# Kernel tuning notes

Hardware: AMD Instinct MI355X
Metric: run time of the kernel (lower is better)

The kernel has to match this reference:

```python
import jax, jax.numpy as jnp
import numpy as np

H, DK = 16, 128  # heads, head dim; d_model = H*DK = 2048

def setup_inputs() -> dict:
    key0 = jax.random.key(0)
    ks = jax.random.split(key0, 11)
    B, S, D = 8, 4096, H * DK
    s = 1.0 / np.sqrt(D)
    return {
        "query": jax.random.normal(ks[0], (B, D), jnp.float32),
        "key": jax.random.normal(ks[1], (S, B, D), jnp.float32),
        "value": jax.random.normal(ks[2], (S, B, D), jnp.float32),
        "Wq": jax.random.normal(ks[3], (D, D), jnp.float32) * s,
        "Wk": jax.random.normal(ks[4], (D, D), jnp.float32) * s,
        "Wv": jax.random.normal(ks[5], (D, D), jnp.float32) * s,
        "bv": jax.random.normal(ks[6], (D,), jnp.float32) * 0.01,
        "Wo": jax.random.normal(ks[7], (D, D), jnp.float32) * s,
        "bo": jax.random.normal(ks[8], (D,), jnp.float32) * 0.01,
        "key_pos": jax.random.normal(ks[9], (4096, H, DK), jnp.float32) * 0.02,
        "q_bias": jax.random.normal(ks[10], (H, DK), jnp.float32) * 0.02,
    }

def reference(query, key, value, Wq, Wk, Wv, bv, Wo, bo, key_pos, q_bias):
    S, B, D = key.shape
    scale = 1.0 / jnp.sqrt(jnp.asarray(DK, query.dtype))
    q = (query @ Wq).reshape(B, H, DK)                 # [B,H,DK]
    k = (key.reshape(S * B, D) @ Wk).reshape(S, B, H, DK)
    v = (value.reshape(S * B, D) @ Wv + bv).reshape(S, B, H, DK)
    kp = key_pos[-S:]                                  # [S,H,DK]
    scores = jnp.einsum('bhd,jbhd->jbh', q + q_bias, k + kp[:, None]) * scale
    attn = jax.nn.softmax(scores, axis=0)              # softmax over seq (dim 0)
    x = jnp.einsum('jbh,jbhd->bhd', attn, v).reshape(B, D)
    return x @ Wo + bo
```

## Files before the change

### kernel.cpp

```cpp
#include <hip/hip_runtime.h>

#define B 8
#define S 4096
#define H 16
#define DK 128
#define D 2048
#define SCALE 0.08838834764831845f

__global__ __launch_bounds__(256) void k0_init(float* __restrict__ qq, float* __restrict__ U,
                                               float* __restrict__ x, float* __restrict__ out,
                                               const float* __restrict__ q_bias,
                                               const float* __restrict__ bv,
                                               const float* __restrict__ bo) {
    int idx = blockIdx.x * 256 + threadIdx.x;
    if (idx < B * D) {
        int d = idx & (D - 1);
        qq[idx]  = q_bias[d];
        x[idx]   = bv[d];
        out[idx] = bo[d];
    }
    if (idx < B * H * D) U[idx] = 0.f;
}

__global__ __launch_bounds__(256) void k1_qproj(const float* __restrict__ query,
                                                const float* __restrict__ Wq,
                                                float* __restrict__ qq) {
    int dout = blockIdx.x * 256 + threadIdx.x;
    int e0 = blockIdx.y * 64;
    float acc[B] = {};
    #pragma unroll 4
    for (int e = e0; e < e0 + 64; ++e) {
        float w = Wq[(size_t)e * D + dout];
        #pragma unroll
        for (int b = 0; b < B; ++b) acc[b] = fmaf(query[b * D + e], w, acc[b]);
    }
    #pragma unroll
    for (int b = 0; b < B; ++b) atomicAdd(&qq[b * D + dout], acc[b]);
}

__global__ __launch_bounds__(256) void k2_A(const float* __restrict__ Wk,
                                            const float* __restrict__ qq,
                                            float* __restrict__ A) {
    int h = blockIdx.x;
    int e = blockIdx.y * 256 + threadIdx.x;
    const float* wrow = Wk + (size_t)e * D + h * DK;
    const float* qb = qq + h * DK;
    float acc[B] = {};
    #pragma unroll 4
    for (int t = 0; t < DK / 4; ++t) {
        float4 w = *(const float4*)(wrow + 4 * t);
        #pragma unroll
        for (int b = 0; b < B; ++b) {
            const float* q4 = qb + b * D + 4 * t;
            acc[b] += w.x * q4[0] + w.y * q4[1] + w.z * q4[2] + w.w * q4[3];
        }
    }
    #pragma unroll
    for (int b = 0; b < B; ++b) A[((size_t)b * H + h) * D + e] = acc[b];
}

__global__ __launch_bounds__(256) void kq_pos(const float* __restrict__ key_pos,
                                              const float* __restrict__ qq,
                                              float* __restrict__ scores) {
    int tid = threadIdx.x;
    int lane = tid & 63;
    int wave = tid >> 6;
    int lane31 = lane & 31;
    int half = lane >> 5;
    for (int t = 0; t < 16; ++t) {
        int task = (blockIdx.x * 4 + wave) * 16 + t;
        int j = task >> 3;
        int hh = task & 7;
        float4 kp4 = *(const float4*)(key_pos + (size_t)j * D + hh * 256 + lane * 4);
        int h = hh * 2 + half;
        #pragma unroll
        for (int b = 0; b < B; ++b) {
            float4 q4 = *(const float4*)(qq + (size_t)b * D + hh * 256 + lane * 4);
            float v = kp4.x * q4.x + kp4.y * q4.y + kp4.z * q4.z + kp4.w * q4.w;
            v += __shfl_xor(v, 1, 64);
            v += __shfl_xor(v, 2, 64);
            v += __shfl_xor(v, 4, 64);
            v += __shfl_xor(v, 8, 64);
            v += __shfl_xor(v, 16, 64);
            if (lane31 == 0) scores[((size_t)b * H + h) * S + j] = v;
        }
    }
}

#define TJ 64
#define EC 128
#define ECF4 32
#define KST 33
__global__ __launch_bounds__(256) void k3_scores(const float* __restrict__ key,
                                                 const float* __restrict__ A,
                                                 float* __restrict__ scores) {
    __shared__ float4 klds[TJ * KST];
    int tid = threadIdx.x;
    int b = blockIdx.y;
    int j0 = blockIdx.x * TJ;
    int jslot = tid & 63;
    int h0 = __builtin_amdgcn_readfirstlane((tid >> 6) << 2);
    const float* Ab = A + ((size_t)b * H + h0) * D;
    float acc0 = 0.f, acc1 = 0.f, acc2 = 0.f, acc3 = 0.f;

    int srow = tid >> 5;
    int scol = tid & 31;
    for (int s = 0; s < D / EC; ++s) {
        __syncthreads();
        const float* gp = key + ((size_t)(j0 + srow) * B + b) * D + s * EC + scol * 4;
        #pragma unroll
        for (int p = 0; p < 8; ++p) {
            klds[(srow + p * 8) * KST + scol] = *(const float4*)(gp + (size_t)p * 8 * B * D);
        }
        __syncthreads();
        const float* Ac = Ab + s * EC;
        #pragma unroll 8
        for (int c = 0; c < ECF4; ++c) {
            float4 k4 = klds[jslot * KST + c];
            float4 a0 = *(const float4*)(Ac + 0 * D + c * 4);
            float4 a1 = *(const float4*)(Ac + 1 * D + c * 4);
            float4 a2 = *(const float4*)(Ac + 2 * D + c * 4);
            float4 a3 = *(const float4*)(Ac + 3 * D + c * 4);
            acc0 += k4.x * a0.x + k4.y * a0.y + k4.z * a0.z + k4.w * a0.w;
            acc1 += k4.x * a1.x + k4.y * a1.y + k4.z * a1.z + k4.w * a1.w;
            acc2 += k4.x * a2.x + k4.y * a2.y + k4.z * a2.z + k4.w * a2.w;
            acc3 += k4.x * a3.x + k4.y * a3.y + k4.z * a3.z + k4.w * a3.w;
        }
    }
    float* sp = scores + ((size_t)b * H + h0) * S + j0 + jslot;
    sp[0 * S] += acc0;
    sp[1 * S] += acc1;
    sp[2 * S] += acc2;
    sp[3 * S] += acc3;
}

__global__ __launch_bounds__(256) void k4_softmax(float* __restrict__ scores) {
    int bh = blockIdx.x;
    float* row = scores + (size_t)bh * S;
    __shared__ float red[4];
    int tid = threadIdx.x, lane = tid & 63, w = tid >> 6;
    float m = -3.0e38f;
    for (int i = tid; i < S; i += 256) m = fmaxf(m, row[i]);
    #pragma unroll
    for (int o = 32; o; o >>= 1) m = fmaxf(m, __shfl_xor(m, o, 64));
    if (lane == 0) red[w] = m;
    __syncthreads();
    float M = fmaxf(fmaxf(red[0], red[1]), fmaxf(red[2], red[3]));
    __syncthreads();
    float s = 0.f;
    for (int i = tid; i < S; i += 256) {
        float e = __expf((row[i] - M) * SCALE);
        row[i] = e;
        s += e;
    }
    #pragma unroll
    for (int o = 32; o; o >>= 1) s += __shfl_xor(s, o, 64);
    if (lane == 0) red[w] = s;
    __syncthreads();
    float inv = 1.f / (red[0] + red[1] + red[2] + red[3]);
    for (int i = tid; i < S; i += 256) row[i] *= inv;
}

__global__ __launch_bounds__(512) void k5_U(const float* __restrict__ value,
                                            const float* __restrict__ attn,
                                            float* __restrict__ U) {
    int tid = threadIdx.x;
    int b = blockIdx.y;
    int j0 = blockIdx.x * 128;
    const float* vbase = value + ((size_t)j0 * B + b) * D + tid * 4;
    float4 acc[H];
    #pragma unroll
    for (int h = 0; h < H; ++h) acc[h] = make_float4(0.f, 0.f, 0.f, 0.f);
    for (int jj = 0; jj < 128; jj += 4) {
        float4 v0 = *(const float4*)(vbase + (size_t)(jj + 0) * B * D);
        float4 v1 = *(const float4*)(vbase + (size_t)(jj + 1) * B * D);
        float4 v2 = *(const float4*)(vbase + (size_t)(jj + 2) * B * D);
        float4 v3 = *(const float4*)(vbase + (size_t)(jj + 3) * B * D);
        #pragma unroll
        for (int h = 0; h < H; ++h) {
            float4 wv = *(const float4*)(attn + ((size_t)b * H + h) * S + j0 + jj);
            acc[h].x += wv.x * v0.x + wv.y * v1.x + wv.z * v2.x + wv.w * v3.x;
            acc[h].y += wv.x * v0.y + wv.y * v1.y + wv.z * v2.y + wv.w * v3.y;
            acc[h].z += wv.x * v0.z + wv.y * v1.z + wv.z * v2.z + wv.w * v3.z;
            acc[h].w += wv.x * v0.w + wv.y * v1.w + wv.z * v2.w + wv.w * v3.w;
        }
    }
    float* ub = U + (size_t)b * H * D + tid * 4;
    #pragma unroll
    for (int h = 0; h < H; ++h) {
        atomicAdd(ub + h * D + 0, acc[h].x);
        atomicAdd(ub + h * D + 1, acc[h].y);
        atomicAdd(ub + h * D + 2, acc[h].z);
        atomicAdd(ub + h * D + 3, acc[h].w);
    }
}

__global__ __launch_bounds__(128) void k6_xv(const float* __restrict__ Wv,
                                             const float* __restrict__ U,
                                             float* __restrict__ x) {
    int d = threadIdx.x;
    int h = blockIdx.y;
    int e0 = blockIdx.x * 32;
    float acc[B] = {};
    #pragma unroll 4
    for (int ee = 0; ee < 32; ++ee) {
        int e = e0 + ee;
        float w = Wv[(size_t)e * D + h * DK + d];
        #pragma unroll
        for (int b = 0; b < B; ++b)
            acc[b] = fmaf(U[((size_t)b * H + h) * D + e], w, acc[b]);
    }
    #pragma unroll
    for (int b = 0; b < B; ++b) atomicAdd(&x[b * D + h * DK + d], acc[b]);
}

__global__ __launch_bounds__(256) void k7_out(const float* __restrict__ x,
                                              const float* __restrict__ Wo,
                                              float* __restrict__ out) {
    int dout = blockIdx.x * 256 + threadIdx.x;
    int e0 = blockIdx.y * 64;
    float acc[B] = {};
    #pragma unroll 4
    for (int e = e0; e < e0 + 64; ++e) {
        float w = Wo[(size_t)e * D + dout];
        #pragma unroll
        for (int b = 0; b < B; ++b) acc[b] = fmaf(x[b * D + e], w, acc[b]);
    }
    #pragma unroll
    for (int b = 0; b < B; ++b) atomicAdd(&out[b * D + dout], acc[b]);
}

extern "C" void kernel_launch(void* const* d_in, const int* in_sizes, int n_in,
                              void* d_out, int out_size, void* d_ws, size_t ws_size,
                              hipStream_t stream) {
    const float* query   = (const float*)d_in[0];
    const float* key     = (const float*)d_in[1];
    const float* value   = (const float*)d_in[2];
    const float* Wq      = (const float*)d_in[3];
    const float* Wk      = (const float*)d_in[4];
    const float* Wv      = (const float*)d_in[5];
    const float* bv      = (const float*)d_in[6];
    const float* Wo      = (const float*)d_in[7];
    const float* bo      = (const float*)d_in[8];
    const float* key_pos = (const float*)d_in[9];
    const float* q_bias  = (const float*)d_in[10];
    float* out = (float*)d_out;

    float* ws     = (float*)d_ws;
    float* qq     = ws;
    float* A      = ws + 16384;
    float* scores = ws + 278528;
    float* U      = ws + 802816;
    float* x      = ws + 1064960;

    hipLaunchKernelGGL(k0_init,    dim3(1024),      dim3(256), 0, stream, qq, U, x, out, q_bias, bv, bo);
    hipLaunchKernelGGL(k1_qproj,   dim3(8, 32),     dim3(256), 0, stream, query, Wq, qq);
    hipLaunchKernelGGL(k2_A,       dim3(16, 8),     dim3(256), 0, stream, Wk, qq, A);
    hipLaunchKernelGGL(kq_pos,     dim3(512),       dim3(256), 0, stream, key_pos, qq, scores);
    hipLaunchKernelGGL(k3_scores,  dim3(64, 8),     dim3(256), 0, stream, key, A, scores);
    hipLaunchKernelGGL(k4_softmax, dim3(128),       dim3(256), 0, stream, scores);
    hipLaunchKernelGGL(k5_U,       dim3(32, 8),     dim3(512), 0, stream, value, scores, U);
    hipLaunchKernelGGL(k6_xv,      dim3(64, 16),    dim3(128), 0, stream, Wv, U, x);
    hipLaunchKernelGGL(k7_out,     dim3(8, 32),     dim3(256), 0, stream, x, Wo, out);
}
```

Before: 894.3 us.

## Replace k5 atomics with partial buffers plus reduction; recast k2_A as wave-per-row

The value-weighted accumulation kernel now writes per-sequence-tile partial sums to a workspace buffer, and a new reduction kernel sums them. This removes the global atomics and the zero-init of U, and the tile count is picked from the available workspace size. Separately, the Wk·q kernel is reorganised so each wave handles one row of Wk with coalesced float4 loads and shuffle reductions, instead of each thread striding across a row. In exchange it adds an extra kernel launch and extra partial-buffer traffic, and with a small workspace the tile count can be low, which limits parallelism.

```diff
diff --git a/kernel.cpp b/kernel.cpp
--- a/kernel.cpp
+++ b/kernel.cpp
@@ -7,7 +7,7 @@
 #define D 2048
 #define SCALE 0.08838834764831845f
 
-__global__ __launch_bounds__(256) void k0_init(float* __restrict__ qq, float* __restrict__ U,
+__global__ __launch_bounds__(256) void k0_init(float* __restrict__ qq,
                                                float* __restrict__ x, float* __restrict__ out,
                                                const float* __restrict__ q_bias,
                                                const float* __restrict__ bv,
@@ -19,7 +19,6 @@
         x[idx]   = bv[d];
         out[idx] = bo[d];
     }
-    if (idx < B * H * D) U[idx] = 0.f;
 }
 
 __global__ __launch_bounds__(256) void k1_qproj(const float* __restrict__ query,
@@ -41,22 +40,27 @@
 __global__ __launch_bounds__(256) void k2_A(const float* __restrict__ Wk,
                                             const float* __restrict__ qq,
                                             float* __restrict__ A) {
-    int h = blockIdx.x;
-    int e = blockIdx.y * 256 + threadIdx.x;
-    const float* wrow = Wk + (size_t)e * D + h * DK;
-    const float* qb = qq + h * DK;
-    float acc[B] = {};
-    #pragma unroll 4
-    for (int t = 0; t < DK / 4; ++t) {
-        float4 w = *(const float4*)(wrow + 4 * t);
+    int tid = threadIdx.x;
+    int lane = tid & 63, wave = tid >> 6;
+    int lane31 = lane & 31, half = lane >> 5;
+    int e = blockIdx.x * 4 + wave;
+    const float* wrow = Wk + (size_t)e * D;
+    #pragma unroll
+    for (int p = 0; p < 8; ++p) {
+        float4 w4 = *(const float4*)(wrow + p * 256 + lane * 4);
+        int h = p * 2 + half;
         #pragma unroll
         for (int b = 0; b < B; ++b) {
-            const float* q4 = qb + b * D + 4 * t;
-            acc[b] += w.x * q4[0] + w.y * q4[1] + w.z * q4[2] + w.w * q4[3];
-        }
-    }
-    #pragma unroll
-    for (int b = 0; b < B; ++b) A[((size_t)b * H + h) * D + e] = acc[b];
+            float4 q4 = *(const float4*)(qq + (size_t)b * D + p * 256 + lane * 4);
+            float v = w4.x * q4.x + w4.y * q4.y + w4.z * q4.z + w4.w * q4.w;
+            v += __shfl_xor(v, 1, 64);
+            v += __shfl_xor(v, 2, 64);
+            v += __shfl_xor(v, 4, 64);
+            v += __shfl_xor(v, 8, 64);
+            v += __shfl_xor(v, 16, 64);
+            if (lane31 == 0) A[((size_t)b * H + h) * D + e] = v;
+        }
+    }
 }
 
 __global__ __launch_bounds__(256) void kq_pos(const float* __restrict__ key_pos,
@@ -163,15 +167,16 @@
 
 __global__ __launch_bounds__(512) void k5_U(const float* __restrict__ value,
                                             const float* __restrict__ attn,
-                                            float* __restrict__ U) {
+                                            float* __restrict__ Upart, int jlen) {
     int tid = threadIdx.x;
     int b = blockIdx.y;
-    int j0 = blockIdx.x * 128;
+    int jt = blockIdx.x;
+    int j0 = jt * jlen;
     const float* vbase = value + ((size_t)j0 * B + b) * D + tid * 4;
     float4 acc[H];
     #pragma unroll
     for (int h = 0; h < H; ++h) acc[h] = make_float4(0.f, 0.f, 0.f, 0.f);
-    for (int jj = 0; jj < 128; jj += 4) {
+    for (int jj = 0; jj < jlen; jj += 4) {
         float4 v0 = *(const float4*)(vbase + (size_t)(jj + 0) * B * D);
         float4 v1 = *(const float4*)(vbase + (size_t)(jj + 1) * B * D);
         float4 v2 = *(const float4*)(vbase + (size_t)(jj + 2) * B * D);
@@ -185,14 +190,21 @@
             acc[h].w += wv.x * v0.w + wv.y * v1.w + wv.z * v2.w + wv.w * v3.w;
         }
     }
-    float* ub = U + (size_t)b * H * D + tid * 4;
-    #pragma unroll
-    for (int h = 0; h < H; ++h) {
-        atomicAdd(ub + h * D + 0, acc[h].x);
-        atomicAdd(ub + h * D + 1, acc[h].y);
-        atomicAdd(ub + h * D + 2, acc[h].z);
-        atomicAdd(ub + h * D + 3, acc[h].w);
-    }
+    float* ub = Upart + (((size_t)jt * B + b) * H) * D + tid * 4;
+    #pragma unroll
+    for (int h = 0; h < H; ++h) *(float4*)(ub + (size_t)h * D) = acc[h];
+}
+
+__global__ __launch_bounds__(256) void k5r(const float* __restrict__ Upart,
+                                           float* __restrict__ U, int JT) {
+    int i = blockIdx.x * 256 + threadIdx.x;
+    float4 s = make_float4(0.f, 0.f, 0.f, 0.f);
+    #pragma unroll 4
+    for (int t = 0; t < JT; ++t) {
+        float4 p = *(const float4*)(Upart + (size_t)t * (B * H * D) + (size_t)i * 4);
+        s.x += p.x; s.y += p.y; s.z += p.z; s.w += p.w;
+    }
+    *(float4*)(U + (size_t)i * 4) = s;
 }
 
 __global__ __launch_bounds__(128) void k6_xv(const float* __restrict__ Wv,
@@ -252,14 +264,23 @@
     float* scores = ws + 278528;
     float* U      = ws + 802816;
     float* x      = ws + 1064960;
-
-    hipLaunchKernelGGL(k0_init,    dim3(1024),      dim3(256), 0, stream, qq, U, x, out, q_bias, bv, bo);
+    float* Upart  = ws + 1081344;
+
+    int JT = 1;
+    for (int cand = 64; cand >= 1; cand >>= 1) {
+        size_t need = ((size_t)1081344 + (size_t)cand * 262144) * sizeof(float);
+        if (need <= ws_size) { JT = cand; break; }
+    }
+    int jlen = S / JT;
+
+    hipLaunchKernelGGL(k0_init,    dim3(64),        dim3(256), 0, stream, qq, x, out, q_bias, bv, bo);
     hipLaunchKernelGGL(k1_qproj,   dim3(8, 32),     dim3(256), 0, stream, query, Wq, qq);
-    hipLaunchKernelGGL(k2_A,       dim3(16, 8),     dim3(256), 0, stream, Wk, qq, A);
+    hipLaunchKernelGGL(k2_A,       dim3(512),       dim3(256), 0, stream, Wk, qq, A);
     hipLaunchKernelGGL(kq_pos,     dim3(512),       dim3(256), 0, stream, key_pos, qq, scores);
     hipLaunchKernelGGL(k3_scores,  dim3(64, 8),     dim3(256), 0, stream, key, A, scores);
     hipLaunchKernelGGL(k4_softmax, dim3(128),       dim3(256), 0, stream, scores);
-    hipLaunchKernelGGL(k5_U,       dim3(32, 8),     dim3(512), 0, stream, value, scores, U);
+    hipLaunchKernelGGL(k5_U,       dim3(JT, 8),     dim3(512), 0, stream, value, scores, Upart, jlen);
+    hipLaunchKernelGGL(k5r,        dim3(256),       dim3(256), 0, stream, Upart, U, JT);
     hipLaunchKernelGGL(k6_xv,      dim3(64, 16),    dim3(128), 0, stream, Wv, U, x);
     hipLaunchKernelGGL(k7_out,     dim3(8, 32),     dim3(256), 0, stream, x, Wo, out);
 }
```

Result: faster. 789.9 us (-11.7%).
